# Optimization experiments

Measured on AMD Instinct MI355X. Metric: run time of the kernel, lower is better.

The kernel has to match this reference:

```python
import jax, jax.numpy as jnp
import numpy as np

N = 500_000          # number of tree nodes
K = 8                # attributes per group
ROWS, COLS = 2048, 4096   # image size; P = ROWS*COLS pixels


def _build_euler_tour(n, seed=0):
    """Random tree (parent[i] < i, parent[0] = 0) + real DFS Euler tour with a
    single timer incremented on both entry (tpre) and exit (tpost)."""
    rng = np.random.default_rng(seed)
    parent = np.zeros(n, dtype=np.int64)
    if n > 1:
        parent[1:] = np.floor(rng.random(n - 1) * np.arange(1, n)).astype(np.int64)
    counts = np.bincount(parent[1:], minlength=n)
    starts = np.zeros(n, dtype=np.int64)
    starts[1:] = np.cumsum(counts)[:-1]
    child_order = np.argsort(parent[1:], kind='stable') + 1  # children grouped by parent
    tpre = np.empty(n, dtype=np.int64)
    tpost = np.empty(n, dtype=np.int64)
    next_child = starts.copy()
    ends = starts + counts
    stack = np.empty(n, dtype=np.int64)
    sp = 0
    stack[0] = 0
    timer = 0
    tpre[0] = timer; timer += 1
    while sp >= 0:
        u = stack[sp]
        if next_child[u] < ends[u]:
            v = child_order[next_child[u]]
            next_child[u] += 1
            sp += 1
            stack[sp] = v
            tpre[v] = timer; timer += 1
        else:
            tpost[u] = timer; timer += 1
            sp -= 1
    return tpre, tpost


def setup_inputs() -> dict:
    key = jax.random.key(0)
    k1, k2, k3, k4 = jax.random.split(key, 4)
    tpre_np, tpost_np = _build_euler_tour(N)
    weight = jax.random.normal(k1, (K,), dtype=jnp.float32) * 0.1
    bias = jnp.zeros((1,), dtype=jnp.float32)
    residues = jax.random.normal(k2, (N,), dtype=jnp.float32)
    attrs2d = jax.random.uniform(k3, (N, K), dtype=jnp.float32)
    node_of_pixel = jax.random.randint(k4, (ROWS * COLS,), 0, N)
    return {
        'weight': weight,
        'bias': bias,
        'residues': residues,
        'attrs2d': attrs2d,
        'tpre': jnp.asarray(tpre_np),
        'tpost': jnp.asarray(tpost_np),
        'node_of_pixel': node_of_pixel,
        'numRows': ROWS,
        'numCols': COLS,
    }


def reference(weight, bias, residues, attrs2d, tpre, tpost, node_of_pixel, numRows, numCols):
    beta_f = 1.0  # module default; clamp_logits=False
    # logits = attrs2d @ w + b ; filtered residues per node
    logits = attrs2d @ weight + bias[0]                     # (N,)
    sig = jax.nn.sigmoid(beta_f * logits)                   # (N,)
    filtered = residues * sig                                # (N,)
    # implicit J.T @ filtered via Euler-tour scatter + prefix scan
    T = 2 * tpre.shape[0]                                    # tpost.max()+1 for a full DFS tour
    delta = (jnp.zeros((T,), dtype=filtered.dtype)
             .at[tpre].add(filtered)
             .at[tpost].add(-filtered))
    y_cumsum = jnp.cumsum(delta)                             # (2N,)
    y = y_cumsum[tpre[node_of_pixel]]                        # (P,) gather per pixel
    return y.reshape(numRows, numCols)
```

## Files before the change

kernel.cpp:

```cpp
#include <hip/hip_runtime.h>

#define SCAN_THREADS 256
#define EPT 8
#define CHUNK (SCAN_THREADS * EPT)

typedef int   v4i __attribute__((ext_vector_type(4)));
typedef float v4f __attribute__((ext_vector_type(4)));

__global__ void k1_filter_scatter(const float* __restrict__ attrs,
                                  const float* __restrict__ weight,
                                  const float* __restrict__ bias,
                                  const float* __restrict__ residues,
                                  const int* __restrict__ tpre,
                                  const int* __restrict__ tpost,
                                  float* __restrict__ delta,
                                  int N) {
    int u0 = (blockIdx.x * blockDim.x + threadIdx.x) * 4;
    v4f w0 = *(const v4f*)weight;
    v4f w1 = *(const v4f*)(weight + 4);
    float b = bias[0];
    if (u0 + 4 <= N) {
        v4f r    = __builtin_nontemporal_load((const v4f*)(residues + u0));
        v4i pre  = *(const v4i*)(tpre + u0);
        v4i post = __builtin_nontemporal_load((const v4i*)(tpost + u0));
        float f[4];
        #pragma unroll
        for (int j = 0; j < 4; ++j) {
            v4f a0 = __builtin_nontemporal_load((const v4f*)(attrs + (size_t)(u0 + j) * 8));
            v4f a1 = __builtin_nontemporal_load((const v4f*)(attrs + (size_t)(u0 + j) * 8 + 4));
            float logit = a0.x*w0.x + a0.y*w0.y + a0.z*w0.z + a0.w*w0.w +
                          a1.x*w1.x + a1.y*w1.y + a1.z*w1.z + a1.w*w1.w + b;
            float sig = 1.0f / (1.0f + __expf(-logit));
            f[j] = r[j] * sig;
        }
        delta[pre.x]  =  f[0]; delta[pre.y]  =  f[1];
        delta[pre.z]  =  f[2]; delta[pre.w]  =  f[3];
        delta[post.x] = -f[0]; delta[post.y] = -f[1];
        delta[post.z] = -f[2]; delta[post.w] = -f[3];
    } else {
        for (int u = u0; u < N; ++u) {
            float logit = b;
            #pragma unroll
            for (int k = 0; k < 8; ++k) logit += attrs[(size_t)u * 8 + k] * weight[k];
            float sig = 1.0f / (1.0f + __expf(-logit));
            float f = residues[u] * sig;
            delta[tpre[u]]  =  f;
            delta[tpost[u]] = -f;
        }
    }
}

__global__ void k2_partials(const float* __restrict__ delta,
                            float* __restrict__ partials, int T) {
    __shared__ float sdata[SCAN_THREADS / 64];
    int base = blockIdx.x * CHUNK + threadIdx.x * EPT;
    float s = 0.0f;
    if (base + EPT <= T) {
        v4f v0 = *(const v4f*)(delta + base);
        v4f v1 = *(const v4f*)(delta + base + 4);
        s = v0.x + v0.y + v0.z + v0.w + v1.x + v1.y + v1.z + v1.w;
    } else {
        for (int i = 0; i < EPT; ++i)
            if (base + i < T) s += delta[base + i];
    }
    #pragma unroll
    for (int d = 32; d > 0; d >>= 1) s += __shfl_down(s, d, 64);
    int lane = threadIdx.x & 63, wid = threadIdx.x >> 6;
    if (lane == 0) sdata[wid] = s;
    __syncthreads();
    if (threadIdx.x == 0) {
        float tot = 0.0f;
        #pragma unroll
        for (int i = 0; i < SCAN_THREADS / 64; ++i) tot += sdata[i];
        partials[blockIdx.x] = tot;
    }
}

__global__ void k3_scan_partials(const float* __restrict__ partials,
                                 float* __restrict__ offsets, int numChunks) {
    int lane = threadIdx.x;
    int ppl = (numChunks + 63) >> 6;
    float s = 0.0f;
    for (int i = 0; i < ppl; ++i) {
        int idx = lane * ppl + i;
        if (idx < numChunks) s += partials[idx];
    }
    float x = s;
    #pragma unroll
    for (int d = 1; d < 64; d <<= 1) {
        float y = __shfl_up(x, d, 64);
        if (lane >= d) x += y;
    }
    float run = x - s;
    for (int i = 0; i < ppl; ++i) {
        int idx = lane * ppl + i;
        if (idx < numChunks) { offsets[idx] = run; run += partials[idx]; }
    }
}

__global__ void k4_scan_chunks(float* __restrict__ data,
                               const float* __restrict__ offsets, int T) {
    __shared__ float wavesums[SCAN_THREADS / 64];
    int base = blockIdx.x * CHUNK + threadIdx.x * EPT;
    float v[EPT];
    bool full = (base + EPT <= T);
    if (full) {
        v4f v0 = *(const v4f*)(data + base);
        v4f v1 = *(const v4f*)(data + base + 4);
        v[0]=v0.x; v[1]=v0.y; v[2]=v0.z; v[3]=v0.w;
        v[4]=v1.x; v[5]=v1.y; v[6]=v1.z; v[7]=v1.w;
    } else {
        for (int i = 0; i < EPT; ++i)
            v[i] = (base + i < T) ? data[base + i] : 0.0f;
    }
    float run = 0.0f;
    #pragma unroll
    for (int i = 0; i < EPT; ++i) { run += v[i]; v[i] = run; }
    float tot = run;
    int lane = threadIdx.x & 63, wid = threadIdx.x >> 6;
    float x = tot;
    #pragma unroll
    for (int d = 1; d < 64; d <<= 1) {
        float y = __shfl_up(x, d, 64);
        if (lane >= d) x += y;
    }
    if (lane == 63) wavesums[wid] = x;
    __syncthreads();
    float woff = 0.0f;
    #pragma unroll
    for (int i = 0; i < SCAN_THREADS / 64; ++i)
        if (i < wid) woff += wavesums[i];
    float add = (x - tot) + woff + offsets[blockIdx.x];
    if (full) {
        v4f o0 = { v[0]+add, v[1]+add, v[2]+add, v[3]+add };
        v4f o1 = { v[4]+add, v[5]+add, v[6]+add, v[7]+add };
        *(v4f*)(data + base)     = o0;
        *(v4f*)(data + base + 4) = o1;
    } else {
        for (int i = 0; i < EPT; ++i)
            if (base + i < T) data[base + i] = v[i] + add;
    }
}

__global__ void k5_node_values(const float* __restrict__ ycum,
                               const int* __restrict__ tpre,
                               float* __restrict__ vnode, int N) {
    int u0 = (blockIdx.x * blockDim.x + threadIdx.x) * 8;
    if (u0 + 8 <= N) {
        v4i t0 = *(const v4i*)(tpre + u0);
        v4i t1 = *(const v4i*)(tpre + u0 + 4);
        v4f o0 = { ycum[t0.x], ycum[t0.y], ycum[t0.z], ycum[t0.w] };
        v4f o1 = { ycum[t1.x], ycum[t1.y], ycum[t1.z], ycum[t1.w] };
        *(v4f*)(vnode + u0)     = o0;
        *(v4f*)(vnode + u0 + 4) = o1;
    } else {
        for (int u = u0; u < N; ++u) vnode[u] = ycum[tpre[u]];
    }
}

__global__ void k6_gather(const float* __restrict__ vnode,
                          const int* __restrict__ nop,
                          float* __restrict__ out, int P) {
    int i = (blockIdx.x * blockDim.x + threadIdx.x) * 16;
    if (i + 16 <= P) {
        v4i n0 = __builtin_nontemporal_load((const v4i*)(nop + i));
        v4i n1 = __builtin_nontemporal_load((const v4i*)(nop + i + 4));
        v4i n2 = __builtin_nontemporal_load((const v4i*)(nop + i + 8));
        v4i n3 = __builtin_nontemporal_load((const v4i*)(nop + i + 12));
        v4f o0 = { vnode[n0.x], vnode[n0.y], vnode[n0.z], vnode[n0.w] };
        v4f o1 = { vnode[n1.x], vnode[n1.y], vnode[n1.z], vnode[n1.w] };
        v4f o2 = { vnode[n2.x], vnode[n2.y], vnode[n2.z], vnode[n2.w] };
        v4f o3 = { vnode[n3.x], vnode[n3.y], vnode[n3.z], vnode[n3.w] };
        *(v4f*)(out + i)      = o0;
        *(v4f*)(out + i + 4)  = o1;
        *(v4f*)(out + i + 8)  = o2;
        *(v4f*)(out + i + 12) = o3;
    } else {
        for (; i < P; ++i) out[i] = vnode[nop[i]];
    }
}

__global__ void k6_direct(const float* __restrict__ ycum,
                          const int* __restrict__ tpre,
                          const int* __restrict__ nop,
                          float* __restrict__ out, int P) {
    int i = (blockIdx.x * blockDim.x + threadIdx.x) * 4;
    if (i + 4 <= P) {
        v4i n = *(const v4i*)(nop + i);
        v4f o = { ycum[tpre[n.x]], ycum[tpre[n.y]], ycum[tpre[n.z]], ycum[tpre[n.w]] };
        *(v4f*)(out + i) = o;
    } else {
        for (; i < P; ++i) out[i] = ycum[tpre[nop[i]]];
    }
}

extern "C" void kernel_launch(void* const* d_in, const int* in_sizes, int n_in,
                              void* d_out, int out_size, void* d_ws, size_t ws_size,
                              hipStream_t stream) {
    const float* weight   = (const float*)d_in[0];
    const float* bias     = (const float*)d_in[1];
    const float* residues = (const float*)d_in[2];
    const float* attrs    = (const float*)d_in[3];
    const int*   tpre     = (const int*)d_in[4];
    const int*   tpost    = (const int*)d_in[5];
    const int*   nop      = (const int*)d_in[6];
    float* out = (float*)d_out;

    const int N = in_sizes[2];
    const int T = 2 * N;
    const int P = out_size;
    const int numChunks = (T + CHUNK - 1) / CHUNK;

    size_t needFull = (size_t)(T + N + 2 * 1024) * sizeof(float);
    size_t needMid  = (size_t)(N + 2 * 1024) * sizeof(float);

    float* delta;
    float* vnode    = nullptr;
    float* partials;
    float* offsets;
    bool useVnode = true;

    if (ws_size >= needFull) {
        delta    = (float*)d_ws;
        vnode    = delta + T;
        partials = vnode + N;
        offsets  = partials + 1024;
    } else if (ws_size >= needMid) {
        delta    = out;
        vnode    = (float*)d_ws;
        partials = vnode + N;
        offsets  = partials + 1024;
    } else {
        delta    = out;
        partials = (float*)d_ws;
        offsets  = partials + 1024;
        useVnode = false;
    }

    k1_filter_scatter<<<(N / 4 + 255) / 256, 256, 0, stream>>>(
        attrs, weight, bias, residues, tpre, tpost, delta, N);
    k2_partials<<<numChunks, SCAN_THREADS, 0, stream>>>(delta, partials, T);
    k3_scan_partials<<<1, 64, 0, stream>>>(partials, offsets, numChunks);
    k4_scan_chunks<<<numChunks, SCAN_THREADS, 0, stream>>>(delta, offsets, T);

    if (useVnode) {
        k5_node_values<<<(N / 8 + 255) / 256, 256, 0, stream>>>(delta, tpre, vnode, N);
        int gatherBlocks = (P / 16 + 255) / 256;
        k6_gather<<<gatherBlocks, 256, 0, stream>>>(vnode, nop, out, P);
    } else {
        int gatherBlocks = (P / 4 + 255) / 256;
        k6_direct<<<gatherBlocks, 256, 0, stream>>>(delta, tpre, nop, out, P);
    }
}
```

Measured before the change: 182.6 us.

## Drop partials-scan kernel, recompute offsets per block, shrink per-thread work

Removes the single-block partial-scan kernel. Each scan block now computes its own offset by reducing all preceding chunk partials, which saves one launch and one serial dependency at the cost of redundant reads of the partials array. Per-thread work is also cut in the filter, node-value and gather kernels, and their nontemporal loads become plain loads. The sigmoid multiply is folded into a single division.

```diff
diff --git a/kernel.cpp b/kernel.cpp
--- a/kernel.cpp
+++ b/kernel.cpp
@@ -15,35 +15,32 @@
                                   const int* __restrict__ tpost,
                                   float* __restrict__ delta,
                                   int N) {
-    int u0 = (blockIdx.x * blockDim.x + threadIdx.x) * 4;
+    int u0 = (blockIdx.x * blockDim.x + threadIdx.x) * 2;
     v4f w0 = *(const v4f*)weight;
     v4f w1 = *(const v4f*)(weight + 4);
     float b = bias[0];
-    if (u0 + 4 <= N) {
-        v4f r    = __builtin_nontemporal_load((const v4f*)(residues + u0));
-        v4i pre  = *(const v4i*)(tpre + u0);
-        v4i post = __builtin_nontemporal_load((const v4i*)(tpost + u0));
-        float f[4];
-        #pragma unroll
-        for (int j = 0; j < 4; ++j) {
-            v4f a0 = __builtin_nontemporal_load((const v4f*)(attrs + (size_t)(u0 + j) * 8));
-            v4f a1 = __builtin_nontemporal_load((const v4f*)(attrs + (size_t)(u0 + j) * 8 + 4));
-            float logit = a0.x*w0.x + a0.y*w0.y + a0.z*w0.z + a0.w*w0.w +
-                          a1.x*w1.x + a1.y*w1.y + a1.z*w1.z + a1.w*w1.w + b;
-            float sig = 1.0f / (1.0f + __expf(-logit));
-            f[j] = r[j] * sig;
-        }
-        delta[pre.x]  =  f[0]; delta[pre.y]  =  f[1];
-        delta[pre.z]  =  f[2]; delta[pre.w]  =  f[3];
-        delta[post.x] = -f[0]; delta[post.y] = -f[1];
-        delta[post.z] = -f[2]; delta[post.w] = -f[3];
+    if (u0 + 2 <= N) {
+        float r0 = residues[u0], r1 = residues[u0 + 1];
+        int pre0 = tpre[u0],  pre1 = tpre[u0 + 1];
+        int pos0 = tpost[u0], pos1 = tpost[u0 + 1];
+        v4f a00 = *(const v4f*)(attrs + (size_t)u0 * 8);
+        v4f a01 = *(const v4f*)(attrs + (size_t)u0 * 8 + 4);
+        v4f a10 = *(const v4f*)(attrs + (size_t)u0 * 8 + 8);
+        v4f a11 = *(const v4f*)(attrs + (size_t)u0 * 8 + 12);
+        float l0 = a00.x*w0.x + a00.y*w0.y + a00.z*w0.z + a00.w*w0.w +
+                   a01.x*w1.x + a01.y*w1.y + a01.z*w1.z + a01.w*w1.w + b;
+        float l1 = a10.x*w0.x + a10.y*w0.y + a10.z*w0.z + a10.w*w0.w +
+                   a11.x*w1.x + a11.y*w1.y + a11.z*w1.z + a11.w*w1.w + b;
+        float f0 = r0 / (1.0f + __expf(-l0));
+        float f1 = r1 / (1.0f + __expf(-l1));
+        delta[pre0] =  f0; delta[pre1] =  f1;
+        delta[pos0] = -f0; delta[pos1] = -f1;
     } else {
         for (int u = u0; u < N; ++u) {
             float logit = b;
             #pragma unroll
             for (int k = 0; k < 8; ++k) logit += attrs[(size_t)u * 8 + k] * weight[k];
-            float sig = 1.0f / (1.0f + __expf(-logit));
-            float f = residues[u] * sig;
+            float f = residues[u] / (1.0f + __expf(-logit));
             delta[tpre[u]]  =  f;
             delta[tpost[u]] = -f;
         }
@@ -68,39 +65,23 @@
     int lane = threadIdx.x & 63, wid = threadIdx.x >> 6;
     if (lane == 0) sdata[wid] = s;
     __syncthreads();
-    if (threadIdx.x == 0) {
-        float tot = 0.0f;
-        #pragma unroll
-        for (int i = 0; i < SCAN_THREADS / 64; ++i) tot += sdata[i];
-        partials[blockIdx.x] = tot;
-    }
-}
-
-__global__ void k3_scan_partials(const float* __restrict__ partials,
-                                 float* __restrict__ offsets, int numChunks) {
-    int lane = threadIdx.x;
-    int ppl = (numChunks + 63) >> 6;
-    float s = 0.0f;
-    for (int i = 0; i < ppl; ++i) {
-        int idx = lane * ppl + i;
-        if (idx < numChunks) s += partials[idx];
-    }
-    float x = s;
-    #pragma unroll
-    for (int d = 1; d < 64; d <<= 1) {
-        float y = __shfl_up(x, d, 64);
-        if (lane >= d) x += y;
-    }
-    float run = x - s;
-    for (int i = 0; i < ppl; ++i) {
-        int idx = lane * ppl + i;
-        if (idx < numChunks) { offsets[idx] = run; run += partials[idx]; }
-    }
+    if (threadIdx.x == 0)
+        partials[blockIdx.x] = sdata[0] + sdata[1] + sdata[2] + sdata[3];
 }
 
 __global__ void k4_scan_chunks(float* __restrict__ data,
-                               const float* __restrict__ offsets, int T) {
+                               const float* __restrict__ partials, int T) {
     __shared__ float wavesums[SCAN_THREADS / 64];
+    __shared__ float redsum[SCAN_THREADS / 64];
+    int lane = threadIdx.x & 63, wid = threadIdx.x >> 6;
+
+    float c = 0.0f;
+    for (int i = threadIdx.x; i < blockIdx.x; i += SCAN_THREADS)
+        c += partials[i];
+    #pragma unroll
+    for (int d = 32; d > 0; d >>= 1) c += __shfl_down(c, d, 64);
+    if (lane == 0) redsum[wid] = c;
+
     int base = blockIdx.x * CHUNK + threadIdx.x * EPT;
     float v[EPT];
     bool full = (base + EPT <= T);
@@ -117,7 +98,6 @@
     #pragma unroll
     for (int i = 0; i < EPT; ++i) { run += v[i]; v[i] = run; }
     float tot = run;
-    int lane = threadIdx.x & 63, wid = threadIdx.x >> 6;
     float x = tot;
     #pragma unroll
     for (int d = 1; d < 64; d <<= 1) {
@@ -126,11 +106,11 @@
     }
     if (lane == 63) wavesums[wid] = x;
     __syncthreads();
-    float woff = 0.0f;
+    float woff = 0.0f, offset = redsum[0] + redsum[1] + redsum[2] + redsum[3];
     #pragma unroll
     for (int i = 0; i < SCAN_THREADS / 64; ++i)
         if (i < wid) woff += wavesums[i];
-    float add = (x - tot) + woff + offsets[blockIdx.x];
+    float add = (x - tot) + woff + offset;
     if (full) {
         v4f o0 = { v[0]+add, v[1]+add, v[2]+add, v[3]+add };
         v4f o1 = { v[4]+add, v[5]+add, v[6]+add, v[7]+add };
@@ -145,14 +125,11 @@
 __global__ void k5_node_values(const float* __restrict__ ycum,
                                const int* __restrict__ tpre,
                                float* __restrict__ vnode, int N) {
-    int u0 = (blockIdx.x * blockDim.x + threadIdx.x) * 8;
-    if (u0 + 8 <= N) {
-        v4i t0 = *(const v4i*)(tpre + u0);
-        v4i t1 = *(const v4i*)(tpre + u0 + 4);
-        v4f o0 = { ycum[t0.x], ycum[t0.y], ycum[t0.z], ycum[t0.w] };
-        v4f o1 = { ycum[t1.x], ycum[t1.y], ycum[t1.z], ycum[t1.w] };
-        *(v4f*)(vnode + u0)     = o0;
-        *(v4f*)(vnode + u0 + 4) = o1;
+    int u0 = (blockIdx.x * blockDim.x + threadIdx.x) * 2;
+    if (u0 + 2 <= N) {
+        int t0 = tpre[u0], t1 = tpre[u0 + 1];
+        float y0 = ycum[t0], y1 = ycum[t1];
+        vnode[u0] = y0; vnode[u0 + 1] = y1;
     } else {
         for (int u = u0; u < N; ++u) vnode[u] = ycum[tpre[u]];
     }
@@ -161,20 +138,14 @@
 __global__ void k6_gather(const float* __restrict__ vnode,
                           const int* __restrict__ nop,
                           float* __restrict__ out, int P) {
-    int i = (blockIdx.x * blockDim.x + threadIdx.x) * 16;
-    if (i + 16 <= P) {
-        v4i n0 = __builtin_nontemporal_load((const v4i*)(nop + i));
-        v4i n1 = __builtin_nontemporal_load((const v4i*)(nop + i + 4));
-        v4i n2 = __builtin_nontemporal_load((const v4i*)(nop + i + 8));
-        v4i n3 = __builtin_nontemporal_load((const v4i*)(nop + i + 12));
+    int i = (blockIdx.x * blockDim.x + threadIdx.x) * 8;
+    if (i + 8 <= P) {
+        v4i n0 = *(const v4i*)(nop + i);
+        v4i n1 = *(const v4i*)(nop + i + 4);
         v4f o0 = { vnode[n0.x], vnode[n0.y], vnode[n0.z], vnode[n0.w] };
         v4f o1 = { vnode[n1.x], vnode[n1.y], vnode[n1.z], vnode[n1.w] };
-        v4f o2 = { vnode[n2.x], vnode[n2.y], vnode[n2.z], vnode[n2.w] };
-        v4f o3 = { vnode[n3.x], vnode[n3.y], vnode[n3.z], vnode[n3.w] };
-        *(v4f*)(out + i)      = o0;
-        *(v4f*)(out + i + 4)  = o1;
-        *(v4f*)(out + i + 8)  = o2;
-        *(v4f*)(out + i + 12) = o3;
+        *(v4f*)(out + i)     = o0;
+        *(v4f*)(out + i + 4) = o1;
     } else {
         for (; i < P; ++i) out[i] = vnode[nop[i]];
     }
@@ -211,41 +182,36 @@
     const int P = out_size;
     const int numChunks = (T + CHUNK - 1) / CHUNK;
 
-    size_t needFull = (size_t)(T + N + 2 * 1024) * sizeof(float);
-    size_t needMid  = (size_t)(N + 2 * 1024) * sizeof(float);
+    size_t needFull = (size_t)(T + N + 1024) * sizeof(float);
+    size_t needMid  = (size_t)(N + 1024) * sizeof(float);
 
     float* delta;
     float* vnode    = nullptr;
     float* partials;
-    float* offsets;
     bool useVnode = true;
 
     if (ws_size >= needFull) {
         delta    = (float*)d_ws;
         vnode    = delta + T;
         partials = vnode + N;
-        offsets  = partials + 1024;
     } else if (ws_size >= needMid) {
         delta    = out;
         vnode    = (float*)d_ws;
         partials = vnode + N;
-        offsets  = partials + 1024;
     } else {
         delta    = out;
         partials = (float*)d_ws;
-        offsets  = partials + 1024;
         useVnode = false;
     }
 
-    k1_filter_scatter<<<(N / 4 + 255) / 256, 256, 0, stream>>>(
+    k1_filter_scatter<<<(N / 2 + 255) / 256, 256, 0, stream>>>(
         attrs, weight, bias, residues, tpre, tpost, delta, N);
     k2_partials<<<numChunks, SCAN_THREADS, 0, stream>>>(delta, partials, T);
-    k3_scan_partials<<<1, 64, 0, stream>>>(partials, offsets, numChunks);
-    k4_scan_chunks<<<numChunks, SCAN_THREADS, 0, stream>>>(delta, offsets, T);
+    k4_scan_chunks<<<numChunks, SCAN_THREADS, 0, stream>>>(delta, partials, T);
 
     if (useVnode) {
-        k5_node_values<<<(N / 8 + 255) / 256, 256, 0, stream>>>(delta, tpre, vnode, N);
-        int gatherBlocks = (P / 16 + 255) / 256;
+        k5_node_values<<<(N / 2 + 255) / 256, 256, 0, stream>>>(delta, tpre, vnode, N);
+        int gatherBlocks = (P / 8 + 255) / 256;
         k6_gather<<<gatherBlocks, 256, 0, stream>>>(vnode, nop, out, P);
     } else {
         int gatherBlocks = (P / 4 + 255) / 256;
```

New measurement: 163.8 us. -10.3%, faster.
